# Optimization experiments

Measured on AMD Instinct MI355X. Metric: run time of the kernel, lower is better.

## Reference

```python
import jax, jax.numpy as jnp
import numpy as np

N = 100000
NFEAT = 128
NHID = 16
HEADS = 8
NCLASS = 40
E = 1600000
NEG_SLOPE = 0.2  # PyG GATConv default


def glorot(key, shape):
    fan = shape[0] + shape[-1]
    limit = float(np.sqrt(6.0 / fan))
    return jax.random.uniform(key, shape, jnp.float32, -limit, limit)


def setup_inputs() -> dict:
    key = jax.random.key(0)
    ks = jax.random.split(key, 10)
    x = jax.random.normal(ks[0], (N, NFEAT), jnp.float32)
    adj = jnp.zeros((1,), jnp.float32)  # unused by forward, kept for signature parity
    edge_index = jax.random.randint(ks[1], (2, E), 0, N, jnp.int64)
    # layer 1: GATConv(NFEAT, NHID, heads=HEADS)
    W1 = glorot(ks[2], (NFEAT, HEADS * NHID))
    att_src1 = glorot(ks[3], (HEADS, NHID))
    att_dst1 = glorot(ks[4], (HEADS, NHID))
    b1 = jnp.zeros((HEADS * NHID,), jnp.float32)
    # layer 2: GATConv(HEADS*NHID, NCLASS, heads=1)
    W2 = glorot(ks[5], (HEADS * NHID, NCLASS))
    att_src2 = glorot(ks[6], (1, NCLASS))
    att_dst2 = glorot(ks[7], (1, NCLASS))
    b2 = jnp.zeros((NCLASS,), jnp.float32)
    return {"x": x, "adj": adj, "edge_index": edge_index,
            "W1": W1, "att_src1": att_src1, "att_dst1": att_dst1, "b1": b1,
            "W2": W2, "att_src2": att_src2, "att_dst2": att_dst2, "b2": b2}


def gat_conv(x, W, att_src, att_dst, bias, src, dst, heads, out_ch):
    n = x.shape[0]
    h = (x @ W).reshape(n, heads, out_ch)              # [N,H,C]
    a_src = (h * att_src[None]).sum(-1)                # [N,H]
    a_dst = (h * att_dst[None]).sum(-1)                # [N,H]
    e = jax.nn.leaky_relu(a_src[src] + a_dst[dst], NEG_SLOPE)  # [E,H]
    # softmax over incoming edges of each destination node
    m = jax.ops.segment_max(e, dst, num_segments=n)
    e = jnp.exp(e - m[dst])
    s = jax.ops.segment_sum(e, dst, num_segments=n)
    alpha = e / s[dst]                                  # [E,H]
    msg = h[src] * alpha[:, :, None]                    # [E,H,C]
    out = jax.ops.segment_sum(msg, dst, num_segments=n)  # [N,H,C]
    return out.reshape(n, heads * out_ch) + bias


def reference(x, adj, edge_index, W1, att_src1, att_dst1, b1, W2, att_src2, att_dst2, b2):
    # PyG GATConv adds self-loops by default
    loops = jnp.arange(N, dtype=edge_index.dtype)
    src = jnp.concatenate([edge_index[0], loops])
    dst = jnp.concatenate([edge_index[1], loops])
    # eval mode: F.dropout is identity
    h = jax.nn.elu(gat_conv(x, W1, att_src1, att_dst1, b1, src, dst, HEADS, NHID))
    h = jax.nn.elu(gat_conv(h, W2, att_src2, att_dst2, b2, src, dst, 1, NCLASS))
    return jax.nn.log_softmax(h, axis=1)
```

## Files before the change

kernel.cpp:

```cpp
#include <hip/hip_runtime.h>
#include <stdint.h>

#define NEG_SLOPE 0.2f

__device__ __forceinline__ float lrelu(float v) { return v >= 0.f ? v : NEG_SLOPE * v; }
__device__ __forceinline__ float elu(float v) { return v > 0.f ? v : expm1f(v); }
__device__ __forceinline__ float pexp(float v) { return __expf(lrelu(v)); }

typedef _Float16 h16x2 __attribute__((ext_vector_type(2)));
typedef _Float16 half8 __attribute__((ext_vector_type(8)));
typedef float floatx4 __attribute__((ext_vector_type(4)));

__device__ __forceinline__ void fma_h2(float& a0, float& a1, float p, unsigned u) {
    h16x2 h = __builtin_bit_cast(h16x2, u);
    a0 += p * (float)h[0];
    a1 += p * (float)h[1];
}


__global__ void prep_kernel(const float* __restrict__ W1, const float* __restrict__ W2,
                            _Float16* __restrict__ w1t, _Float16* __restrict__ w2t,
                            int* __restrict__ deg, int n) {
    int t = blockIdx.x * 256 + threadIdx.x;
    if (t < n) deg[t] = 0;
    if (t < 128 * 128) {
        int col = t >> 7, k = t & 127;
        w1t[col * 128 + k] = (_Float16)W1[k * 128 + col];
    }
    if (t < 48 * 128) {
        int col = t >> 7, k = t & 127;
        w2t[t] = (col < 40) ? (_Float16)W2[k * 40 + col] : (_Float16)0.f;
    }
}


__global__ __launch_bounds__(256) void hist_gemm1_kernel(
    const int* __restrict__ ei, int* __restrict__ deg, unsigned* __restrict__ rankd,
    const float* __restrict__ x, const _Float16* __restrict__ w1t,
    const float* __restrict__ as1, const float* __restrict__ ad1,
    _Float16* __restrict__ h1h, float* __restrict__ a1s, float* __restrict__ a1d,
    int E, int n, int nbh) {
    const int b = blockIdx.x;
    const int tid = threadIdx.x;
    if (b < nbh) {
        int e = b * 256 + tid;
        if (e >= E) return;
        int d = ei[E + e];
        unsigned rd = 0xFFFFFFFFu;
        if ((unsigned)d < (unsigned)n) {
            int r = atomicAdd(&deg[d], 1);
            rd = ((unsigned)d << 7) | (unsigned)r;
        }
        rankd[e] = rd;
        return;
    }
    const int bg = b - nbh;
    const int wave = tid >> 6, lane = tid & 63;
    const int cl = lane & 15, g = lane >> 4;
    const int wbase = bg * 64 + wave * 16;

    int arow = wbase + cl;
    if (arow >= n) arow = n - 1;
    half8 afr[4];
    #pragma unroll
    for (int t = 0; t < 4; t++) {
        const float4 v0 = *(const float4*)&x[(size_t)arow * 128 + 32 * t + g * 8];
        const float4 v1 = *(const float4*)&x[(size_t)arow * 128 + 32 * t + g * 8 + 4];
        afr[t][0] = (_Float16)v0.x; afr[t][1] = (_Float16)v0.y;
        afr[t][2] = (_Float16)v0.z; afr[t][3] = (_Float16)v0.w;
        afr[t][4] = (_Float16)v1.x; afr[t][5] = (_Float16)v1.y;
        afr[t][6] = (_Float16)v1.z; afr[t][7] = (_Float16)v1.w;
    }

    #pragma unroll
    for (int ct = 0; ct < 8; ct++) {
        const int col = ct * 16 + cl;
        half8 bfr[4];
        #pragma unroll
        for (int t = 0; t < 4; t++)
            bfr[t] = *(const half8*)&w1t[col * 128 + 32 * t + 8 * g];
        floatx4 acc = {0.f, 0.f, 0.f, 0.f};
        #pragma unroll
        for (int t = 0; t < 4; t++)
            acc = __builtin_amdgcn_mfma_f32_16x16x32_f16(afr[t], bfr[t], acc, 0, 0, 0);
        const float av = as1[col], dv = ad1[col];
        #pragma unroll
        for (int i = 0; i < 4; i++) {
            int r = wbase + g * 4 + i;
            float hv = acc[i];
            if (r < n) h1h[(size_t)r * 128 + col] = (_Float16)hv;
            float ps = hv * av, pd = hv * dv;
            ps += __shfl_xor(ps, 1); ps += __shfl_xor(ps, 2);
            ps += __shfl_xor(ps, 4); ps += __shfl_xor(ps, 8);
            pd += __shfl_xor(pd, 1); pd += __shfl_xor(pd, 2);
            pd += __shfl_xor(pd, 4); pd += __shfl_xor(pd, 8);
            if (cl == 0 && r < n) {
                a1s[r * 8 + ct] = ps;
                a1d[r * 8 + ct] = pd;
            }
        }
    }
}


#define SCAN_T 256
#define SCAN_TILE 1024

__global__ __launch_bounds__(SCAN_T) void scan_p1_kernel(const int* __restrict__ deg,
                                                         int* __restrict__ bsum, int n) {
    __shared__ int red[SCAN_T];
    int t = threadIdx.x;
    int base = blockIdx.x * SCAN_TILE + t * 4;
    int s = 0;
    #pragma unroll
    for (int i = 0; i < 4; i++) {
        int idx = base + i;
        if (idx < n) s += deg[idx];
    }
    red[t] = s;
    __syncthreads();
    for (int off = SCAN_T / 2; off; off >>= 1) {
        if (t < off) red[t] += red[t + off];
        __syncthreads();
    }
    if (t == 0) bsum[blockIdx.x] = red[0];
}

__global__ __launch_bounds__(1024) void scan_p2_kernel(int* __restrict__ bsum, int nb,
                                                       int* __restrict__ total) {
    __shared__ int sh[1024];
    int t = threadIdx.x;
    int v = (t < nb) ? bsum[t] : 0;
    sh[t] = v;
    __syncthreads();
    for (int off = 1; off < 1024; off <<= 1) {
        int add = (t >= off) ? sh[t - off] : 0;
        __syncthreads();
        sh[t] += add;
        __syncthreads();
    }
    if (t < nb) bsum[t] = sh[t] - v;
    if (t == nb - 1) *total = sh[t];
}

__global__ __launch_bounds__(SCAN_T) void scan_p3_kernel(const int* __restrict__ deg,
                                                         const int* __restrict__ bsum,
                                                         int* __restrict__ row_ptr, int n) {
    __shared__ int red[SCAN_T];
    int t = threadIdx.x;
    int base = blockIdx.x * SCAN_TILE + t * 4;
    int v[4];
    int s = 0;
    #pragma unroll
    for (int i = 0; i < 4; i++) {
        int idx = base + i;
        v[i] = (idx < n) ? deg[idx] : 0;
        s += v[i];
    }
    red[t] = s;
    __syncthreads();
    for (int off = 1; off < SCAN_T; off <<= 1) {
        int add = (t >= off) ? red[t - off] : 0;
        __syncthreads();
        red[t] += add;
        __syncthreads();
    }
    int excl = red[t] - s + bsum[blockIdx.x];
    #pragma unroll
    for (int i = 0; i < 4; i++) {
        int idx = base + i;
        if (idx < n) row_ptr[idx] = excl;
        excl += v[i];
    }
}

__global__ void scatter_kernel(const int* __restrict__ ei, const unsigned* __restrict__ rankd,
                               const int* __restrict__ row_ptr,
                               int* __restrict__ csr_src, int E) {
    int e = blockIdx.x * blockDim.x + threadIdx.x;
    if (e >= E) return;
    unsigned rd = rankd[e];
    if (rd == 0xFFFFFFFFu) return;
    int d = (int)(rd >> 7), r = (int)(rd & 127u);
    csr_src[row_ptr[d] + r] = ei[e];
}


__global__ __launch_bounds__(256) void agg1_kernel(const int* __restrict__ row_ptr,
                                                   const int* __restrict__ csr_src,
                                                   const float* __restrict__ a1s,
                                                   const float* __restrict__ a1d,
                                                   const uint4* __restrict__ h1q,
                                                   const float* __restrict__ b1,
                                                   _Float16* __restrict__ h2h, int n) {
    int lane = threadIdx.x & 63;
    int d = blockIdx.x * 4 + (threadIdx.x >> 6);
    if (d >= n) return;
    const int g = lane >> 4;
    const int q = lane & 15;
    const int h = q >> 1;
    const float adh = a1d[d * 8 + h];

    float acc[8];
    #pragma unroll
    for (int i = 0; i < 8; i++) acc[i] = 0.f;
    float sum = 0.f;
    if (g == 0) {
        uint4 w = h1q[(size_t)d * 16 + q];
        float ps = pexp(a1s[d * 8 + h] + adh);
        fma_h2(acc[0], acc[1], ps, w.x);
        fma_h2(acc[2], acc[3], ps, w.y);
        fma_h2(acc[4], acc[5], ps, w.z);
        fma_h2(acc[6], acc[7], ps, w.w);
        sum = ps;
    }
    int beg = row_ptr[d], end = row_ptr[d + 1];
    int e = beg + g;
    for (; e + 12 < end; e += 16) {
        int s0 = csr_src[e],     s1 = csr_src[e + 4];
        int s2 = csr_src[e + 8], s3 = csr_src[e + 12];
        uint4 w0 = h1q[(size_t)s0 * 16 + q];
        uint4 w1 = h1q[(size_t)s1 * 16 + q];
        uint4 w2 = h1q[(size_t)s2 * 16 + q];
        uint4 w3 = h1q[(size_t)s3 * 16 + q];
        float p0 = pexp(a1s[s0 * 8 + h] + adh);
        float p1 = pexp(a1s[s1 * 8 + h] + adh);
        float p2 = pexp(a1s[s2 * 8 + h] + adh);
        float p3 = pexp(a1s[s3 * 8 + h] + adh);
        fma_h2(acc[0], acc[1], p0, w0.x); fma_h2(acc[2], acc[3], p0, w0.y);
        fma_h2(acc[4], acc[5], p0, w0.z); fma_h2(acc[6], acc[7], p0, w0.w);
        fma_h2(acc[0], acc[1], p1, w1.x); fma_h2(acc[2], acc[3], p1, w1.y);
        fma_h2(acc[4], acc[5], p1, w1.z); fma_h2(acc[6], acc[7], p1, w1.w);
        fma_h2(acc[0], acc[1], p2, w2.x); fma_h2(acc[2], acc[3], p2, w2.y);
        fma_h2(acc[4], acc[5], p2, w2.z); fma_h2(acc[6], acc[7], p2, w2.w);
        fma_h2(acc[0], acc[1], p3, w3.x); fma_h2(acc[2], acc[3], p3, w3.y);
        fma_h2(acc[4], acc[5], p3, w3.z); fma_h2(acc[6], acc[7], p3, w3.w);
        sum += (p0 + p1) + (p2 + p3);
    }
    for (; e + 4 < end; e += 8) {
        int s0 = csr_src[e], s1 = csr_src[e + 4];
        uint4 w0 = h1q[(size_t)s0 * 16 + q];
        uint4 w1 = h1q[(size_t)s1 * 16 + q];
        float p0 = pexp(a1s[s0 * 8 + h] + adh);
        float p1 = pexp(a1s[s1 * 8 + h] + adh);
        fma_h2(acc[0], acc[1], p0, w0.x); fma_h2(acc[2], acc[3], p0, w0.y);
        fma_h2(acc[4], acc[5], p0, w0.z); fma_h2(acc[6], acc[7], p0, w0.w);
        fma_h2(acc[0], acc[1], p1, w1.x); fma_h2(acc[2], acc[3], p1, w1.y);
        fma_h2(acc[4], acc[5], p1, w1.z); fma_h2(acc[6], acc[7], p1, w1.w);
        sum += p0 + p1;
    }
    for (; e < end; e += 4) {
        int s = csr_src[e];
        uint4 w = h1q[(size_t)s * 16 + q];
        float p = pexp(a1s[s * 8 + h] + adh);
        fma_h2(acc[0], acc[1], p, w.x);
        fma_h2(acc[2], acc[3], p, w.y);
        fma_h2(acc[4], acc[5], p, w.z);
        fma_h2(acc[6], acc[7], p, w.w);
        sum += p;
    }
    sum += __shfl_xor(sum, 16); sum += __shfl_xor(sum, 32);
    #pragma unroll
    for (int i = 0; i < 8; i++) {
        acc[i] += __shfl_xor(acc[i], 16);
        acc[i] += __shfl_xor(acc[i], 32);
    }
    if (g == 0) {
        float rs = 1.f / sum;
        float4 b0 = *(const float4*)&b1[8 * q];
        float4 b4 = *(const float4*)&b1[8 * q + 4];
        half8 o;
        o[0] = (_Float16)elu(acc[0] * rs + b0.x);
        o[1] = (_Float16)elu(acc[1] * rs + b0.y);
        o[2] = (_Float16)elu(acc[2] * rs + b0.z);
        o[3] = (_Float16)elu(acc[3] * rs + b0.w);
        o[4] = (_Float16)elu(acc[4] * rs + b4.x);
        o[5] = (_Float16)elu(acc[5] * rs + b4.y);
        o[6] = (_Float16)elu(acc[6] * rs + b4.z);
        o[7] = (_Float16)elu(acc[7] * rs + b4.w);
        *(half8*)&h2h[(size_t)d * 128 + 8 * q] = o;
    }
}


__global__ __launch_bounds__(256) void gemm2_mfma_kernel(
    const _Float16* __restrict__ h2h, const _Float16* __restrict__ w2t,
    const float* __restrict__ as2, const float* __restrict__ ad2,
    _Float16* __restrict__ h3pk, float* __restrict__ a2d, int n) {
    const int tid = threadIdx.x;
    const int wave = tid >> 6, lane = tid & 63;
    const int cl = lane & 15, g = lane >> 4;
    const int wbase = blockIdx.x * 64 + wave * 16;

    int arow = wbase + cl;
    if (arow >= n) arow = n - 1;
    half8 afr[4];
    #pragma unroll
    for (int t = 0; t < 4; t++)
        afr[t] = *(const half8*)&h2h[(size_t)arow * 128 + 32 * t + 8 * g];

    float ps[4] = {0.f, 0.f, 0.f, 0.f};
    float pd[4] = {0.f, 0.f, 0.f, 0.f};
    #pragma unroll
    for (int ct = 0; ct < 3; ct++) {
        const int col = ct * 16 + cl;
        half8 bfr[4];
        #pragma unroll
        for (int t = 0; t < 4; t++)
            bfr[t] = *(const half8*)&w2t[col * 128 + 32 * t + 8 * g];
        floatx4 acc = {0.f, 0.f, 0.f, 0.f};
        #pragma unroll
        for (int t = 0; t < 4; t++)
            acc = __builtin_amdgcn_mfma_f32_16x16x32_f16(afr[t], bfr[t], acc, 0, 0, 0);
        const bool cv = (col < 40);
        const float av = cv ? as2[col] : 0.f;
        const float dv = cv ? ad2[col] : 0.f;
        #pragma unroll
        for (int i = 0; i < 4; i++) {
            int r = wbase + g * 4 + i;
            float hv = acc[i];
            if (cv && r < n)
                h3pk[(size_t)r * 64 + 2 + col] = (_Float16)hv;
            ps[i] += hv * av;
            pd[i] += hv * dv;
        }
    }
    #pragma unroll
    for (int i = 0; i < 4; i++) {
        float s = ps[i], dd = pd[i];
        s += __shfl_xor(s, 1); s += __shfl_xor(s, 2);
        s += __shfl_xor(s, 4); s += __shfl_xor(s, 8);
        dd += __shfl_xor(dd, 1); dd += __shfl_xor(dd, 2);
        dd += __shfl_xor(dd, 4); dd += __shfl_xor(dd, 8);
        int r = wbase + g * 4 + i;
        if (cl == 0 && r < n) {
            ((float*)h3pk)[(size_t)r * 32] = s;
            a2d[r] = dd;
        }
    }
}

__global__ __launch_bounds__(256) void agg2_final_kernel(const int* __restrict__ row_ptr,
                                                         const int* __restrict__ csr_src,
                                                         const unsigned* __restrict__ h3u,
                                                         const float* __restrict__ a2d,
                                                         const float* __restrict__ b2,
                                                         float* __restrict__ out, int n) {
    const float* h3a = (const float*)h3u;
    int lane = threadIdx.x & 63;
    int d = blockIdx.x * 4 + (threadIdx.x >> 6);
    if (d >= n) return;
    const int g = lane >> 5;
    const int q = lane & 31;
    const bool act = (q < 20);
    const float adh = a2d[d];

    h16x2 hsel = {(_Float16)0.f, (_Float16)0.f};
    if (act && g == 0) hsel = __builtin_bit_cast(h16x2, h3u[(size_t)d * 32 + 1 + q]);

    float acc0 = 0.f, acc1 = 0.f, sum = 0.f;
    if (g == 0) {
        float ps = pexp(h3a[(size_t)d * 32] + adh);
        acc0 = ps * (float)hsel[0]; acc1 = ps * (float)hsel[1]; sum = ps;
    }
    int beg = row_ptr[d], end = row_ptr[d + 1];
    int e = beg + g;
    for (; e + 14 < end; e += 16) {
        int s0 = csr_src[e],      s1 = csr_src[e + 2];
        int s2 = csr_src[e + 4],  s3 = csr_src[e + 6];
        int s4 = csr_src[e + 8],  s5 = csr_src[e + 10];
        int s6 = csr_src[e + 12], s7 = csr_src[e + 14];
        float a0 = h3a[(size_t)s0 * 32], a1 = h3a[(size_t)s1 * 32];
        float a2 = h3a[(size_t)s2 * 32], a3 = h3a[(size_t)s3 * 32];
        float a4 = h3a[(size_t)s4 * 32], a5 = h3a[(size_t)s5 * 32];
        float a6 = h3a[(size_t)s6 * 32], a7 = h3a[(size_t)s7 * 32];
        unsigned w0 = 0u, w1 = 0u, w2 = 0u, w3 = 0u;
        unsigned w4 = 0u, w5 = 0u, w6 = 0u, w7 = 0u;
        if (act) {
            w0 = h3u[(size_t)s0 * 32 + 1 + q]; w1 = h3u[(size_t)s1 * 32 + 1 + q];
            w2 = h3u[(size_t)s2 * 32 + 1 + q]; w3 = h3u[(size_t)s3 * 32 + 1 + q];
            w4 = h3u[(size_t)s4 * 32 + 1 + q]; w5 = h3u[(size_t)s5 * 32 + 1 + q];
            w6 = h3u[(size_t)s6 * 32 + 1 + q]; w7 = h3u[(size_t)s7 * 32 + 1 + q];
        }
        float p0 = pexp(a0 + adh), p1 = pexp(a1 + adh);
        float p2 = pexp(a2 + adh), p3 = pexp(a3 + adh);
        float p4 = pexp(a4 + adh), p5 = pexp(a5 + adh);
        float p6 = pexp(a6 + adh), p7 = pexp(a7 + adh);
        fma_h2(acc0, acc1, p0, w0); fma_h2(acc0, acc1, p1, w1);
        fma_h2(acc0, acc1, p2, w2); fma_h2(acc0, acc1, p3, w3);
        fma_h2(acc0, acc1, p4, w4); fma_h2(acc0, acc1, p5, w5);
        fma_h2(acc0, acc1, p6, w6); fma_h2(acc0, acc1, p7, w7);
        sum += ((p0 + p1) + (p2 + p3)) + ((p4 + p5) + (p6 + p7));
    }
    for (; e < end; e += 2) {
        int s = csr_src[e];
        float pe = pexp(h3a[(size_t)s * 32] + adh);
        unsigned w = act ? h3u[(size_t)s * 32 + 1 + q] : 0u;
        fma_h2(acc0, acc1, pe, w);
        sum += pe;
    }
    sum += __shfl_xor(sum, 32);
    acc0 += __shfl_xor(acc0, 32);
    acc1 += __shfl_xor(acc1, 32);

    float rs = 1.f / sum;
    float v0 = -3.0e38f, v1 = -3.0e38f;
    if (act) {
        v0 = elu(acc0 * rs + b2[2 * q]);
        v1 = elu(acc1 * rs + b2[2 * q + 1]);
    }
    float mx = (act && g == 0) ? fmaxf(v0, v1) : -3.0e38f;
    #pragma unroll
    for (int off = 32; off; off >>= 1) mx = fmaxf(mx, __shfl_xor(mx, off, 64));
    float es = (act && g == 0) ? (__expf(v0 - mx) + __expf(v1 - mx)) : 0.f;
    #pragma unroll
    for (int off = 32; off; off >>= 1) es += __shfl_xor(es, off, 64);
    if (act && g == 0) {
        float ls = logf(es);
        float2 o;
        o.x = v0 - mx - ls;
        o.y = v1 - mx - ls;
        *(float2*)&out[(size_t)d * 40 + 2 * q] = o;
    }
}

extern "C" void kernel_launch(void* const* d_in, const int* in_sizes, int n_in,
                              void* d_out, int out_size, void* d_ws, size_t ws_size,
                              hipStream_t stream) {
    const float* x   = (const float*)d_in[0];
    const int*   ei  = (const int*)d_in[2];
    const float* W1  = (const float*)d_in[3];
    const float* as1 = (const float*)d_in[4];
    const float* ad1 = (const float*)d_in[5];
    const float* b1  = (const float*)d_in[6];
    const float* W2  = (const float*)d_in[7];
    const float* as2 = (const float*)d_in[8];
    const float* ad2 = (const float*)d_in[9];
    const float* b2  = (const float*)d_in[10];
    float* out = (float*)d_out;

    const int n = in_sizes[0] / 128;
    const int E = in_sizes[2] / 2;
    const int nb = (n + SCAN_TILE - 1) / SCAN_TILE;
    const int nbh = (E + 255) / 256;
    const int nbg = (n + 63) / 64;

    float* ws = (float*)d_ws;
    _Float16* h1h = (_Float16*)ws;
    _Float16* h2h = (_Float16*)(ws + (size_t)n * 64);
    float* A  = ws + (size_t)n * 128;
    int* deg    = (int*)A;
    int* bsum   = deg + n;
    float* a1s = A;
    float* a1d = A + (size_t)n * 8;
    float* a2d = A;
    int* row_ptr = (int*)(A + (size_t)n * 16);
    int* csr_src = row_ptr + (n + 1);
    unsigned* rankd = (unsigned*)(csr_src + E);
    _Float16* w1t = (_Float16*)(((uintptr_t)(rankd + E) + 63) & ~(uintptr_t)63);
    _Float16* w2t = w1t + 128 * 128;
    _Float16* h3pk = h1h;

    deg  = (int*)(w2t + 48 * 128);
    bsum = deg + n;

    prep_kernel<<<(n + 255) / 256, 256, 0, stream>>>(W1, W2, w1t, w2t, deg, n);
    hist_gemm1_kernel<<<nbh + nbg, 256, 0, stream>>>(ei, deg, rankd, x, w1t, as1, ad1,
                                                     h1h, a1s, a1d, E, n, nbh);
    scan_p1_kernel<<<nb, SCAN_T, 0, stream>>>(deg, bsum, n);
    scan_p2_kernel<<<1, 1024, 0, stream>>>(bsum, nb, &row_ptr[n]);
    scan_p3_kernel<<<nb, SCAN_T, 0, stream>>>(deg, bsum, row_ptr, n);
    scatter_kernel<<<(E + 255) / 256, 256, 0, stream>>>(ei, rankd, row_ptr, csr_src, E);

    agg1_kernel<<<(n + 3) / 4, 256, 0, stream>>>(row_ptr, csr_src, a1s, a1d,
                                                 (const uint4*)h1h, b1, h2h, n);

    gemm2_mfma_kernel<<<(n + 63) / 64, 256, 0, stream>>>(h2h, w2t, as2, ad2, h3pk, a2d, n);
    agg2_final_kernel<<<(n + 3) / 4, 256, 0, stream>>>(row_ptr, csr_src, (const unsigned*)h3pk,
                                                       a2d, b2, out, n);
}
```

Baseline: 439.3 us.

## Split GEMM1 from histogram, vectorize edge histogram and scatter by four

The degree histogram now runs in a kernel that also transposes W1/W2. The first-layer GEMM moves into its own kernel launched after the CSR build, and deg is zeroed with hipMemsetAsync instead of a prep kernel. The histogram and scatter kernels each handle four edges per thread with int4/uint4 loads to cut per-edge load overhead. This removes the old fusion of GEMM1 with the histogram, which was needed because the histogram previously read w1t produced by the prep kernel. It assumes E is a multiple of 4 and 16-byte alignment for the vector loads, and changes the workspace layout padding.

```diff
diff --git a/kernel.cpp b/kernel.cpp
--- a/kernel.cpp
+++ b/kernel.cpp
@@ -18,46 +18,143 @@
 }
 
 
-__global__ void prep_kernel(const float* __restrict__ W1, const float* __restrict__ W2,
-                            _Float16* __restrict__ w1t, _Float16* __restrict__ w2t,
-                            int* __restrict__ deg, int n) {
-    int t = blockIdx.x * 256 + threadIdx.x;
-    if (t < n) deg[t] = 0;
-    if (t < 128 * 128) {
-        int col = t >> 7, k = t & 127;
-        w1t[col * 128 + k] = (_Float16)W1[k * 128 + col];
-    }
-    if (t < 48 * 128) {
-        int col = t >> 7, k = t & 127;
-        w2t[t] = (col < 40) ? (_Float16)W2[k * 40 + col] : (_Float16)0.f;
-    }
-}
-
-
-__global__ __launch_bounds__(256) void hist_gemm1_kernel(
-    const int* __restrict__ ei, int* __restrict__ deg, unsigned* __restrict__ rankd,
-    const float* __restrict__ x, const _Float16* __restrict__ w1t,
-    const float* __restrict__ as1, const float* __restrict__ ad1,
-    _Float16* __restrict__ h1h, float* __restrict__ a1s, float* __restrict__ a1d,
-    int E, int n, int nbh) {
+__global__ __launch_bounds__(256) void hist_wt_kernel(const int* __restrict__ ei,
+                                                      int* __restrict__ deg,
+                                                      unsigned* __restrict__ rankd,
+                                                      const float* __restrict__ W1,
+                                                      const float* __restrict__ W2,
+                                                      _Float16* __restrict__ w1t,
+                                                      _Float16* __restrict__ w2t,
+                                                      int E, int n, int nbh) {
     const int b = blockIdx.x;
     const int tid = threadIdx.x;
     if (b < nbh) {
-        int e = b * 256 + tid;
-        if (e >= E) return;
-        int d = ei[E + e];
-        unsigned rd = 0xFFFFFFFFu;
-        if ((unsigned)d < (unsigned)n) {
-            int r = atomicAdd(&deg[d], 1);
-            rd = ((unsigned)d << 7) | (unsigned)r;
+        int e0 = (b * 256 + tid) * 4;
+        if (e0 >= E) return;
+        int4 d4 = *(const int4*)&ei[E + e0];
+        unsigned r0 = 0xFFFFFFFFu, r1 = 0xFFFFFFFFu, r2 = 0xFFFFFFFFu, r3 = 0xFFFFFFFFu;
+        if ((unsigned)d4.x < (unsigned)n)
+            r0 = ((unsigned)d4.x << 7) | (unsigned)atomicAdd(&deg[d4.x], 1);
+        if ((unsigned)d4.y < (unsigned)n)
+            r1 = ((unsigned)d4.y << 7) | (unsigned)atomicAdd(&deg[d4.y], 1);
+        if ((unsigned)d4.z < (unsigned)n)
+            r2 = ((unsigned)d4.z << 7) | (unsigned)atomicAdd(&deg[d4.z], 1);
+        if ((unsigned)d4.w < (unsigned)n)
+            r3 = ((unsigned)d4.w << 7) | (unsigned)atomicAdd(&deg[d4.w], 1);
+        uint4 rv; rv.x = r0; rv.y = r1; rv.z = r2; rv.w = r3;
+        *(uint4*)&rankd[e0] = rv;
+        return;
+    }
+    if (b < nbh + 64) {
+        int t = (b - nbh) * 256 + tid;
+        int col = t >> 7, k = t & 127;
+        w1t[col * 128 + k] = (_Float16)W1[k * 128 + col];
+        return;
+    }
+    {
+        int t = (b - nbh - 64) * 256 + tid;
+        if (t < 48 * 128) {
+            int col = t >> 7, k = t & 127;
+            w2t[t] = (col < 40) ? (_Float16)W2[k * 40 + col] : (_Float16)0.f;
         }
-        rankd[e] = rd;
-        return;
-    }
-    const int bg = b - nbh;
+    }
+}
+
+
+#define SCAN_T 256
+#define SCAN_TILE 1024
+
+__global__ __launch_bounds__(SCAN_T) void scan_p1_kernel(const int* __restrict__ deg,
+                                                         int* __restrict__ bsum, int n) {
+    __shared__ int red[SCAN_T];
+    int t = threadIdx.x;
+    int base = blockIdx.x * SCAN_TILE + t * 4;
+    int s = 0;
+    #pragma unroll
+    for (int i = 0; i < 4; i++) {
+        int idx = base + i;
+        if (idx < n) s += deg[idx];
+    }
+    red[t] = s;
+    __syncthreads();
+    for (int off = SCAN_T / 2; off; off >>= 1) {
+        if (t < off) red[t] += red[t + off];
+        __syncthreads();
+    }
+    if (t == 0) bsum[blockIdx.x] = red[0];
+}
+
+__global__ __launch_bounds__(1024) void scan_p2_kernel(int* __restrict__ bsum, int nb,
+                                                       int* __restrict__ total) {
+    __shared__ int sh[1024];
+    int t = threadIdx.x;
+    int v = (t < nb) ? bsum[t] : 0;
+    sh[t] = v;
+    __syncthreads();
+    for (int off = 1; off < 1024; off <<= 1) {
+        int add = (t >= off) ? sh[t - off] : 0;
+        __syncthreads();
+        sh[t] += add;
+        __syncthreads();
+    }
+    if (t < nb) bsum[t] = sh[t] - v;
+    if (t == nb - 1) *total = sh[t];
+}
+
+__global__ __launch_bounds__(SCAN_T) void scan_p3_kernel(const int* __restrict__ deg,
+                                                         const int* __restrict__ bsum,
+                                                         int* __restrict__ row_ptr, int n) {
+    __shared__ int red[SCAN_T];
+    int t = threadIdx.x;
+    int base = blockIdx.x * SCAN_TILE + t * 4;
+    int v[4];
+    int s = 0;
+    #pragma unroll
+    for (int i = 0; i < 4; i++) {
+        int idx = base + i;
+        v[i] = (idx < n) ? deg[idx] : 0;
+        s += v[i];
+    }
+    red[t] = s;
+    __syncthreads();
+    for (int off = 1; off < SCAN_T; off <<= 1) {
+        int add = (t >= off) ? red[t - off] : 0;
+        __syncthreads();
+        red[t] += add;
+        __syncthreads();
+    }
+    int excl = red[t] - s + bsum[blockIdx.x];
+    #pragma unroll
+    for (int i = 0; i < 4; i++) {
+        int idx = base + i;
+        if (idx < n) row_ptr[idx] = excl;
+        excl += v[i];
+    }
+}
+
+__global__ __launch_bounds__(256) void scatter4_kernel(const int* __restrict__ ei,
+                                                       const unsigned* __restrict__ rankd,
+                                                       const int* __restrict__ row_ptr,
+                                                       int* __restrict__ csr_src, int E) {
+    int e0 = (blockIdx.x * 256 + threadIdx.x) * 4;
+    if (e0 >= E) return;
+    int4 s4 = *(const int4*)&ei[e0];
+    uint4 r4 = *(const uint4*)&rankd[e0];
+    if (r4.x != 0xFFFFFFFFu) csr_src[row_ptr[r4.x >> 7] + (int)(r4.x & 127u)] = s4.x;
+    if (r4.y != 0xFFFFFFFFu) csr_src[row_ptr[r4.y >> 7] + (int)(r4.y & 127u)] = s4.y;
+    if (r4.z != 0xFFFFFFFFu) csr_src[row_ptr[r4.z >> 7] + (int)(r4.z & 127u)] = s4.z;
+    if (r4.w != 0xFFFFFFFFu) csr_src[row_ptr[r4.w >> 7] + (int)(r4.w & 127u)] = s4.w;
+}
+
+
+__global__ __launch_bounds__(256) void gemm1_mfma_kernel(
+    const float* __restrict__ x, const _Float16* __restrict__ w1t,
+    const float* __restrict__ as1, const float* __restrict__ ad1,
+    _Float16* __restrict__ h1h, float* __restrict__ a1s, float* __restrict__ a1d, int n) {
+    const int tid = threadIdx.x;
     const int wave = tid >> 6, lane = tid & 63;
     const int cl = lane & 15, g = lane >> 4;
-    const int wbase = bg * 64 + wave * 16;
+    const int wbase = blockIdx.x * 64 + wave * 16;
 
     int arow = wbase + cl;
     if (arow >= n) arow = n - 1;
@@ -101,90 +198,6 @@
         }
     }
 }
-
-
-#define SCAN_T 256
-#define SCAN_TILE 1024
-
-__global__ __launch_bounds__(SCAN_T) void scan_p1_kernel(const int* __restrict__ deg,
-                                                         int* __restrict__ bsum, int n) {
-    __shared__ int red[SCAN_T];
-    int t = threadIdx.x;
-    int base = blockIdx.x * SCAN_TILE + t * 4;
-    int s = 0;
-    #pragma unroll
-    for (int i = 0; i < 4; i++) {
-        int idx = base + i;
-        if (idx < n) s += deg[idx];
-    }
-    red[t] = s;
-    __syncthreads();
-    for (int off = SCAN_T / 2; off; off >>= 1) {
-        if (t < off) red[t] += red[t + off];
-        __syncthreads();
-    }
-    if (t == 0) bsum[blockIdx.x] = red[0];
-}
-
-__global__ __launch_bounds__(1024) void scan_p2_kernel(int* __restrict__ bsum, int nb,
-                                                       int* __restrict__ total) {
-    __shared__ int sh[1024];
-    int t = threadIdx.x;
-    int v = (t < nb) ? bsum[t] : 0;
-    sh[t] = v;
-    __syncthreads();
-    for (int off = 1; off < 1024; off <<= 1) {
-        int add = (t >= off) ? sh[t - off] : 0;
-        __syncthreads();
-        sh[t] += add;
-        __syncthreads();
-    }
-    if (t < nb) bsum[t] = sh[t] - v;
-    if (t == nb - 1) *total = sh[t];
-}
-
-__global__ __launch_bounds__(SCAN_T) void scan_p3_kernel(const int* __restrict__ deg,
-                                                         const int* __restrict__ bsum,
-                                                         int* __restrict__ row_ptr, int n) {
-    __shared__ int red[SCAN_T];
-    int t = threadIdx.x;
-    int base = blockIdx.x * SCAN_TILE + t * 4;
-    int v[4];
-    int s = 0;
-    #pragma unroll
-    for (int i = 0; i < 4; i++) {
-        int idx = base + i;
-        v[i] = (idx < n) ? deg[idx] : 0;
-        s += v[i];
-    }
-    red[t] = s;
-    __syncthreads();
-    for (int off = 1; off < SCAN_T; off <<= 1) {
-        int add = (t >= off) ? red[t - off] : 0;
-        __syncthreads();
-        red[t] += add;
-        __syncthreads();
-    }
-    int excl = red[t] - s + bsum[blockIdx.x];
-    #pragma unroll
-    for (int i = 0; i < 4; i++) {
-        int idx = base + i;
-        if (idx < n) row_ptr[idx] = excl;
-        excl += v[i];
-    }
-}
-
-__global__ void scatter_kernel(const int* __restrict__ ei, const unsigned* __restrict__ rankd,
-                               const int* __restrict__ row_ptr,
-                               int* __restrict__ csr_src, int E) {
-    int e = blockIdx.x * blockDim.x + threadIdx.x;
-    if (e >= E) return;
-    unsigned rd = rankd[e];
-    if (rd == 0xFFFFFFFFu) return;
-    int d = (int)(rd >> 7), r = (int)(rd & 127u);
-    csr_src[row_ptr[d] + r] = ei[e];
-}
-
 
 __global__ __launch_bounds__(256) void agg1_kernel(const int* __restrict__ row_ptr,
                                                    const int* __restrict__ csr_src,
@@ -442,36 +455,33 @@
     const int n = in_sizes[0] / 128;
     const int E = in_sizes[2] / 2;
     const int nb = (n + SCAN_TILE - 1) / SCAN_TILE;
-    const int nbh = (E + 255) / 256;
-    const int nbg = (n + 63) / 64;
+    const int nbh4 = (E + 1023) / 1024;
 
     float* ws = (float*)d_ws;
     _Float16* h1h = (_Float16*)ws;
     _Float16* h2h = (_Float16*)(ws + (size_t)n * 64);
     float* A  = ws + (size_t)n * 128;
-    int* deg    = (int*)A;
-    int* bsum   = deg + n;
     float* a1s = A;
     float* a1d = A + (size_t)n * 8;
     float* a2d = A;
     int* row_ptr = (int*)(A + (size_t)n * 16);
-    int* csr_src = row_ptr + (n + 1);
+    int* csr_src = row_ptr + (n + 4);
     unsigned* rankd = (unsigned*)(csr_src + E);
-    _Float16* w1t = (_Float16*)(((uintptr_t)(rankd + E) + 63) & ~(uintptr_t)63);
+    _Float16* w1t = (_Float16*)(rankd + E);
     _Float16* w2t = w1t + 128 * 128;
+    int* deg  = (int*)(w2t + 48 * 128);
+    int* bsum = deg + n;
     _Float16* h3pk = h1h;
 
-    deg  = (int*)(w2t + 48 * 128);
-    bsum = deg + n;
-
-    prep_kernel<<<(n + 255) / 256, 256, 0, stream>>>(W1, W2, w1t, w2t, deg, n);
-    hist_gemm1_kernel<<<nbh + nbg, 256, 0, stream>>>(ei, deg, rankd, x, w1t, as1, ad1,
-                                                     h1h, a1s, a1d, E, n, nbh);
+    hipMemsetAsync(deg, 0, (size_t)n * sizeof(int), stream);
+    hist_wt_kernel<<<nbh4 + 64 + 24, 256, 0, stream>>>(ei, deg, rankd, W1, W2,
+                                                       w1t, w2t, E, n, nbh4);
     scan_p1_kernel<<<nb, SCAN_T, 0, stream>>>(deg, bsum, n);
     scan_p2_kernel<<<1, 1024, 0, stream>>>(bsum, nb, &row_ptr[n]);
     scan_p3_kernel<<<nb, SCAN_T, 0, stream>>>(deg, bsum, row_ptr, n);
-    scatter_kernel<<<(E + 255) / 256, 256, 0, stream>>>(ei, rankd, row_ptr, csr_src, E);
-
+    scatter4_kernel<<<nbh4, 256, 0, stream>>>(ei, rankd, row_ptr, csr_src, E);
+
+    gemm1_mfma_kernel<<<(n + 63) / 64, 256, 0, stream>>>(x, w1t, as1, ad1, h1h, a1s, a1d, n);
     agg1_kernel<<<(n + 3) / 4, 256, 0, stream>>>(row_ptr, csr_src, a1s, a1d,
                                                  (const uint4*)h1h, b1, h2h, n);
 
```

Measured after the change: 441.9 us. About the same (+0.6%).
